# Kernel optimization log

Measured on AMD Instinct MI355X. Metric: run time of the kernel, lower is better.

## Reference

```python
import jax, jax.numpy as jnp
import numpy as np

N = 100_000  # nodes
E = 1_600_000  # edges (before self-loops)
NEG_SLOPE = 0.2  # PyG GATConv default leaky_relu slope


def gat_layer(x, W, a_src, a_dst, b, src, dst, heads, out_ch, concat):
    # x: [N, Fin]; W: [Fin, heads*out_ch]; a_src/a_dst: [1, heads, out_ch]
    h = (x @ W).reshape(-1, heads, out_ch)            # [N, H, C]
    alpha_s = jnp.sum(h * a_src, axis=-1)             # [N, H]
    alpha_d = jnp.sum(h * a_dst, axis=-1)             # [N, H]
    e = jax.nn.leaky_relu(alpha_s[src] + alpha_d[dst], NEG_SLOPE)  # [E', H]
    # softmax over edges grouped by destination node (self-loops guarantee
    # every node has at least one incoming edge)
    m = jax.ops.segment_max(e, dst, num_segments=N)   # [N, H]
    p = jnp.exp(e - m[dst])                           # [E', H]
    s = jax.ops.segment_sum(p, dst, num_segments=N)   # [N, H]
    alpha = p / s[dst]                                # [E', H]
    out = jax.ops.segment_sum(alpha[:, :, None] * h[src], dst, num_segments=N)  # [N,H,C]
    out = out.reshape(-1, heads * out_ch) if concat else out.mean(axis=1)
    return out + b


def setup_inputs() -> dict:
    key = jax.random.key(0)
    ks = jax.random.split(key, 8)

    def glorot(k, shape):
        return (jax.random.normal(k, shape, jnp.float32) / np.sqrt(np.float32(shape[0]))).astype(jnp.float32)

    x = jax.random.normal(ks[0], (N, 512), jnp.float32)
    edge_index = jax.random.randint(ks[1], (2, E), 0, N, dtype=jnp.int64)
    W1 = glorot(ks[2], (512, 64))
    att_src1 = jax.random.normal(ks[3], (1, 8, 8), jnp.float32) * 0.1
    att_dst1 = jax.random.normal(ks[4], (1, 8, 8), jnp.float32) * 0.1
    b1 = jnp.zeros((64,), jnp.float32)
    W2 = glorot(ks[5], (64, 128))
    att_src2 = jax.random.normal(ks[6], (1, 1, 128), jnp.float32) * 0.1
    att_dst2 = jax.random.normal(ks[7], (1, 1, 128), jnp.float32) * 0.1
    b2 = jnp.zeros((128,), jnp.float32)
    return {"x": x, "edge_index": edge_index, "W1": W1, "att_src1": att_src1,
            "att_dst1": att_dst1, "b1": b1, "W2": W2, "att_src2": att_src2,
            "att_dst2": att_dst2, "b2": b2}


def reference(x, edge_index, W1, att_src1, att_dst1, b1, W2, att_src2, att_dst2, b2):
    # PyG GATConv adds self-loops by default
    loop = jnp.arange(N, dtype=edge_index.dtype)
    src = jnp.concatenate([edge_index[0], loop])
    dst = jnp.concatenate([edge_index[1], loop])
    h = gat_layer(x, W1, att_src1, att_dst1, b1, src, dst, heads=8, out_ch=8, concat=True)
    h = jax.nn.elu(h)
    z = gat_layer(h, W2, att_src2, att_dst2, b2, src, dst, heads=1, out_ch=128, concat=False)
    return z
```

## Files before the change

kernel.cpp:

```cpp
#include <hip/hip_runtime.h>
#include <math.h>

#define NNODES 100000

__device__ __forceinline__ float lrelu(float v) { return v > 0.f ? v : 0.2f * v; }

__global__ __launch_bounds__(256) void gemm1_k(const float* __restrict__ x,
                                               const float* __restrict__ W,
                                               float* __restrict__ h1, int Nn) {
    __shared__ float xs[64][132];
    __shared__ float ws[64][68];
    int r0 = blockIdx.x * 128;
    int t = threadIdx.x;
    int ty = t >> 4, tx = t & 15;
    float acc[8][4] = {};
    for (int kb = 0; kb < 512; kb += 64) {
        for (int l = t; l < 2048; l += 256) {
            int row = l >> 4;
            int c4 = (l & 15) * 4;
            int gr = r0 + row;
            float4 v = make_float4(0.f, 0.f, 0.f, 0.f);
            if (gr < Nn) v = *reinterpret_cast<const float4*>(&x[(size_t)gr * 512 + kb + c4]);
            xs[c4][row] = v.x; xs[c4 + 1][row] = v.y; xs[c4 + 2][row] = v.z; xs[c4 + 3][row] = v.w;
        }
        for (int l = t; l < 1024; l += 256) {
            int row = l >> 4;
            int c4 = (l & 15) * 4;
            *reinterpret_cast<float4*>(&ws[row][c4]) =
                *reinterpret_cast<const float4*>(&W[(size_t)(kb + row) * 64 + c4]);
        }
        __syncthreads();
#pragma unroll 4
        for (int k = 0; k < 64; ++k) {
            float4 a0 = *reinterpret_cast<const float4*>(&xs[k][ty * 8]);
            float4 a1 = *reinterpret_cast<const float4*>(&xs[k][ty * 8 + 4]);
            float4 bv = *reinterpret_cast<const float4*>(&ws[k][tx * 4]);
            float a[8] = {a0.x, a0.y, a0.z, a0.w, a1.x, a1.y, a1.z, a1.w};
            float b[4] = {bv.x, bv.y, bv.z, bv.w};
#pragma unroll
            for (int i = 0; i < 8; ++i)
#pragma unroll
                for (int j = 0; j < 4; ++j) acc[i][j] += a[i] * b[j];
        }
        __syncthreads();
    }
#pragma unroll
    for (int i = 0; i < 8; ++i) {
        int gr = r0 + ty * 8 + i;
        if (gr < Nn) {
            float4 o = make_float4(acc[i][0], acc[i][1], acc[i][2], acc[i][3]);
            *reinterpret_cast<float4*>(&h1[(size_t)gr * 64 + tx * 4]) = o;
        }
    }
}

__global__ __launch_bounds__(256) void gemm2_k(const float* __restrict__ xin,
                                               const float* __restrict__ W,
                                               float* __restrict__ h2, int Nn) {
    __shared__ float xs[64][68];
    __shared__ float ws[64][132];
    int r0 = blockIdx.x * 64;
    int t = threadIdx.x;
    int ty = t >> 4, tx = t & 15;
    for (int l = t; l < 1024; l += 256) {
        int row = l >> 4;
        int c4 = (l & 15) * 4;
        int gr = r0 + row;
        float4 v = make_float4(0.f, 0.f, 0.f, 0.f);
        if (gr < Nn) v = *reinterpret_cast<const float4*>(&xin[(size_t)gr * 64 + c4]);
        xs[c4][row] = v.x; xs[c4 + 1][row] = v.y; xs[c4 + 2][row] = v.z; xs[c4 + 3][row] = v.w;
    }
    for (int l = t; l < 2048; l += 256) {
        int row = l >> 5;
        int c4 = (l & 31) * 4;
        *reinterpret_cast<float4*>(&ws[row][c4]) =
            *reinterpret_cast<const float4*>(&W[(size_t)row * 128 + c4]);
    }
    __syncthreads();
    float acc0[4][4] = {};
    float acc1[4][4] = {};
#pragma unroll 4
    for (int k = 0; k < 64; ++k) {
        float4 av = *reinterpret_cast<const float4*>(&xs[k][ty * 4]);
        float4 b0v = *reinterpret_cast<const float4*>(&ws[k][tx * 4]);
        float4 b1v = *reinterpret_cast<const float4*>(&ws[k][64 + tx * 4]);
        float a[4] = {av.x, av.y, av.z, av.w};
        float b0[4] = {b0v.x, b0v.y, b0v.z, b0v.w};
        float b1[4] = {b1v.x, b1v.y, b1v.z, b1v.w};
#pragma unroll
        for (int i = 0; i < 4; ++i)
#pragma unroll
            for (int j = 0; j < 4; ++j) {
                acc0[i][j] += a[i] * b0[j];
                acc1[i][j] += a[i] * b1[j];
            }
    }
#pragma unroll
    for (int i = 0; i < 4; ++i) {
        int gr = r0 + ty * 4 + i;
        if (gr < Nn) {
            float4 o0 = make_float4(acc0[i][0], acc0[i][1], acc0[i][2], acc0[i][3]);
            float4 o1 = make_float4(acc1[i][0], acc1[i][1], acc1[i][2], acc1[i][3]);
            *reinterpret_cast<float4*>(&h2[(size_t)gr * 128 + tx * 4]) = o0;
            *reinterpret_cast<float4*>(&h2[(size_t)gr * 128 + 64 + tx * 4]) = o1;
        }
    }
}

__global__ __launch_bounds__(256) void attn1_k(const float* __restrict__ h1,
                                               const float* __restrict__ asrc,
                                               const float* __restrict__ adst,
                                               float* __restrict__ as1,
                                               float* __restrict__ ad1, int Nn) {
    int t = blockIdx.x * 256 + threadIdx.x;
    int n = t >> 3, h = t & 7;
    if (n >= Nn) return;
    const float* hp = h1 + (size_t)n * 64 + h * 8;
    float s = 0.f, d = 0.f;
#pragma unroll
    for (int c = 0; c < 8; ++c) {
        float v = hp[c];
        s += v * asrc[h * 8 + c];
        d += v * adst[h * 8 + c];
    }
    as1[(size_t)n * 8 + h] = s;
    ad1[(size_t)n * 8 + h] = d;
}

__global__ __launch_bounds__(256) void attn2_k(const float* __restrict__ h2,
                                               const float* __restrict__ asrc,
                                               const float* __restrict__ adst,
                                               float* __restrict__ as2,
                                               float* __restrict__ ad2, int Nn) {
    int wid = threadIdx.x >> 6, lane = threadIdx.x & 63;
    int n = blockIdx.x * 4 + wid;
    if (n >= Nn) return;
    float v0 = h2[(size_t)n * 128 + lane];
    float v1 = h2[(size_t)n * 128 + 64 + lane];
    float s = v0 * asrc[lane] + v1 * asrc[64 + lane];
    float d = v0 * adst[lane] + v1 * adst[64 + lane];
#pragma unroll
    for (int off = 32; off >= 1; off >>= 1) {
        s += __shfl_xor(s, off);
        d += __shfl_xor(d, off);
    }
    if (lane == 0) { as2[n] = s; ad2[n] = d; }
}

__global__ __launch_bounds__(256) void hist_k(const int* __restrict__ ei, int E, int Etot,
                                              int* __restrict__ indeg) {
    int e = blockIdx.x * 256 + threadIdx.x;
    if (e >= Etot) return;
    int d = (e < E) ? ei[E + e] : (e - E);
    atomicAdd(&indeg[d], 1);
}

__global__ __launch_bounds__(256) void scanA_k(const int* __restrict__ indeg,
                                               int* __restrict__ indptr,
                                               int* __restrict__ bsums, int Nn) {
    __shared__ int sd[256];
    int t = threadIdx.x;
    int i0 = blockIdx.x * 2048 + t * 8;
    int v[8], ex[8];
    int run = 0;
#pragma unroll
    for (int j = 0; j < 8; ++j) {
        int i = i0 + j;
        v[j] = (i < Nn) ? indeg[i] : 0;
        ex[j] = run;
        run += v[j];
    }
    sd[t] = run;
    __syncthreads();
    for (int off = 1; off < 256; off <<= 1) {
        int a = (t >= off) ? sd[t - off] : 0;
        __syncthreads();
        sd[t] += a;
        __syncthreads();
    }
    int texc = sd[t] - run;
#pragma unroll
    for (int j = 0; j < 8; ++j) {
        int i = i0 + j;
        if (i < Nn) indptr[i] = texc + ex[j];
    }
    if (t == 0) bsums[blockIdx.x] = sd[255];
}

__global__ void scanB_k(int* __restrict__ bsums, int nb) {
    if (threadIdx.x == 0 && blockIdx.x == 0) {
        int run = 0;
        for (int b = 0; b < nb; ++b) {
            int x = bsums[b];
            bsums[b] = run;
            run += x;
        }
    }
}

__global__ __launch_bounds__(256) void scanC_k(int* __restrict__ indptr,
                                               const int* __restrict__ bsums,
                                               int* __restrict__ cursor, int Nn, int Etot) {
    int t = threadIdx.x;
    int b = blockIdx.x;
    int base = bsums[b];
    int i0 = b * 2048 + t * 8;
#pragma unroll
    for (int j = 0; j < 8; ++j) {
        int i = i0 + j;
        if (i < Nn) {
            int val = indptr[i] + base;
            indptr[i] = val;
            cursor[i] = val;
        }
    }
    if (b == 0 && t == 0) indptr[Nn] = Etot;
}

__global__ __launch_bounds__(256) void fill_k(const int* __restrict__ ei, int E, int Etot,
                                              int* __restrict__ cursor, int* __restrict__ col) {
    int e = blockIdx.x * 256 + threadIdx.x;
    if (e >= Etot) return;
    int s, d;
    if (e < E) { s = ei[e]; d = ei[E + e]; }
    else { s = e - E; d = e - E; }
    int pos = atomicAdd(&cursor[d], 1);
    col[pos] = s;
}

__global__ __launch_bounds__(256) void agg1_k(const float* __restrict__ h1,
                                              const float* __restrict__ as1,
                                              const float* __restrict__ ad1,
                                              const int* __restrict__ indptr,
                                              const int* __restrict__ col,
                                              const float* __restrict__ b1,
                                              float* __restrict__ h1a, int Nn) {
    int wid = threadIdx.x >> 6, lane = threadIdx.x & 63;
    int n = blockIdx.x * 4 + wid;
    if (n >= Nn) return;
    int beg = indptr[n], end = indptr[n + 1];
    int h = lane & 7, eo = lane >> 3;
    float adn = ad1[(size_t)n * 8 + h];
    float ss = 0.f;
    for (int i = beg + eo; i < end; i += 8) {
        int s = col[i];
        ss += __expf(lrelu(as1[(size_t)s * 8 + h] + adn));
    }
    ss += __shfl_xor(ss, 8);
    ss += __shfl_xor(ss, 16);
    ss += __shfl_xor(ss, 32);
    int hb = lane >> 3;
    float sb = __shfl(ss, hb);
    float ab = __shfl(adn, hb);
    float inv = 1.f / sb;
    const float* __restrict__ h1l = h1 + lane;
    float acc0 = 0.f, acc1 = 0.f, acc2 = 0.f, acc3 = 0.f;
    int i = beg;
    for (; i + 4 <= end; i += 4) {
        int s0 = col[i], s1 = col[i + 1], s2 = col[i + 2], s3 = col[i + 3];
        float w0 = __expf(lrelu(as1[(size_t)s0 * 8 + hb] + ab));
        float w1 = __expf(lrelu(as1[(size_t)s1 * 8 + hb] + ab));
        float w2 = __expf(lrelu(as1[(size_t)s2 * 8 + hb] + ab));
        float w3 = __expf(lrelu(as1[(size_t)s3 * 8 + hb] + ab));
        acc0 += w0 * h1l[(size_t)s0 * 64];
        acc1 += w1 * h1l[(size_t)s1 * 64];
        acc2 += w2 * h1l[(size_t)s2 * 64];
        acc3 += w3 * h1l[(size_t)s3 * 64];
    }
    for (; i < end; ++i) {
        int s = col[i];
        acc0 += __expf(lrelu(as1[(size_t)s * 8 + hb] + ab)) * h1l[(size_t)s * 64];
    }
    float o = ((acc0 + acc1) + (acc2 + acc3)) * inv + b1[lane];
    h1a[(size_t)n * 64 + lane] = o > 0.f ? o : expm1f(o);
}

__global__ __launch_bounds__(256) void agg2_k(const float* __restrict__ h2,
                                              const float* __restrict__ as2,
                                              const float* __restrict__ ad2,
                                              const int* __restrict__ indptr,
                                              const int* __restrict__ col,
                                              const float* __restrict__ b2,
                                              float* __restrict__ out, int Nn) {
    int wid = threadIdx.x >> 6, lane = threadIdx.x & 63;
    int n = blockIdx.x * 4 + wid;
    if (n >= Nn) return;
    int beg = indptr[n], end = indptr[n + 1];
    float adn = ad2[n];
    float ss = 0.f;
    for (int i = beg + lane; i < end; i += 64) {
        ss += __expf(lrelu(as2[col[i]] + adn));
    }
#pragma unroll
    for (int off = 32; off >= 1; off >>= 1) ss += __shfl_xor(ss, off);
    float inv = 1.f / ss;
    const float* __restrict__ h2l = h2 + lane;
    float a00 = 0.f, a01 = 0.f, a02 = 0.f, a03 = 0.f;
    float a10 = 0.f, a11 = 0.f, a12 = 0.f, a13 = 0.f;
    int i = beg;
    for (; i + 4 <= end; i += 4) {
        int s0 = col[i], s1 = col[i + 1], s2 = col[i + 2], s3 = col[i + 3];
        float w0 = __expf(lrelu(as2[s0] + adn));
        float w1 = __expf(lrelu(as2[s1] + adn));
        float w2 = __expf(lrelu(as2[s2] + adn));
        float w3 = __expf(lrelu(as2[s3] + adn));
        a00 += w0 * h2l[(size_t)s0 * 128];
        a10 += w0 * h2l[(size_t)s0 * 128 + 64];
        a01 += w1 * h2l[(size_t)s1 * 128];
        a11 += w1 * h2l[(size_t)s1 * 128 + 64];
        a02 += w2 * h2l[(size_t)s2 * 128];
        a12 += w2 * h2l[(size_t)s2 * 128 + 64];
        a03 += w3 * h2l[(size_t)s3 * 128];
        a13 += w3 * h2l[(size_t)s3 * 128 + 64];
    }
    for (; i < end; ++i) {
        int s = col[i];
        float w = __expf(lrelu(as2[s] + adn));
        a00 += w * h2l[(size_t)s * 128];
        a10 += w * h2l[(size_t)s * 128 + 64];
    }
    out[(size_t)n * 128 + lane] = ((a00 + a01) + (a02 + a03)) * inv + b2[lane];
    out[(size_t)n * 128 + 64 + lane] = ((a10 + a11) + (a12 + a13)) * inv + b2[64 + lane];
}

extern "C" void kernel_launch(void* const* d_in, const int* in_sizes, int n_in,
                              void* d_out, int out_size, void* d_ws, size_t ws_size,
                              hipStream_t stream) {
    const float* x = (const float*)d_in[0];
    const int* ei = (const int*)d_in[1];
    const float* W1 = (const float*)d_in[2];
    const float* asrc1 = (const float*)d_in[3];
    const float* adst1 = (const float*)d_in[4];
    const float* b1 = (const float*)d_in[5];
    const float* W2 = (const float*)d_in[6];
    const float* asrc2 = (const float*)d_in[7];
    const float* adst2 = (const float*)d_in[8];
    const float* b2 = (const float*)d_in[9];
    float* out = (float*)d_out;

    const int Nn = NNODES;
    const int E = in_sizes[1] / 2;
    const int Etot = E + Nn;

    char* w = (char*)d_ws;
    auto alloc = [&](size_t bytes) {
        char* p = w;
        w += (bytes + 255) & ~(size_t)255;
        return p;
    };
    float* h1 = (float*)alloc((size_t)Nn * 64 * 4);
    float* h1a = (float*)alloc((size_t)Nn * 64 * 4);
    float* h2 = (float*)alloc((size_t)Nn * 128 * 4);
    float* as1 = (float*)alloc((size_t)Nn * 8 * 4);
    float* ad1 = (float*)alloc((size_t)Nn * 8 * 4);
    float* as2 = (float*)alloc((size_t)Nn * 4);
    float* ad2 = (float*)alloc((size_t)Nn * 4);
    int* indeg = (int*)alloc((size_t)(Nn + 1) * 4);
    int* indptr = (int*)alloc((size_t)(Nn + 1) * 4);
    int* cursor = (int*)alloc((size_t)Nn * 4);
    int* bsums = (int*)alloc(4096);
    int* col = (int*)alloc((size_t)Etot * 4);

    const int NBLK = (Nn + 2047) / 2048;

    hipMemsetAsync(indeg, 0, (size_t)Nn * 4, stream);
    gemm1_k<<<(Nn + 127) / 128, 256, 0, stream>>>(x, W1, h1, Nn);
    attn1_k<<<(Nn * 8 + 255) / 256, 256, 0, stream>>>(h1, asrc1, adst1, as1, ad1, Nn);
    hist_k<<<(Etot + 255) / 256, 256, 0, stream>>>(ei, E, Etot, indeg);
    scanA_k<<<NBLK, 256, 0, stream>>>(indeg, indptr, bsums, Nn);
    scanB_k<<<1, 64, 0, stream>>>(bsums, NBLK);
    scanC_k<<<NBLK, 256, 0, stream>>>(indptr, bsums, cursor, Nn, Etot);
    fill_k<<<(Etot + 255) / 256, 256, 0, stream>>>(ei, E, Etot, cursor, col);
    agg1_k<<<(Nn + 3) / 4, 256, 0, stream>>>(h1, as1, ad1, indptr, col, b1, h1a, Nn);
    gemm2_k<<<(Nn + 63) / 64, 256, 0, stream>>>(h1a, W2, h2, Nn);
    attn2_k<<<(Nn + 3) / 4, 256, 0, stream>>>(h2, asrc2, adst2, as2, ad2, Nn);
    agg2_k<<<(Nn + 3) / 4, 256, 0, stream>>>(h2, as2, ad2, indptr, col, b2, out, Nn);
}
```

Measured before the change: 877.9 us.

## Retile both GEMMs with swizzled row-major LDS and unroll aggregation loops by eight

The x and hidden tiles are now stored row-major in LDS with an XOR swizzle, which replaces the transposed scalar stores. Each thread now computes an 8x8 output tile, and gemm1 runs with 128 threads per block while gemm2 handles 128 rows per block. The two edge-aggregation kernels unroll their gather loop from four to eight edges, keeping more independent loads in flight. This adds register pressure, which could lower occupancy, and the larger gemm2 blocks reduce the number of blocks launched.

Result: slower. 1.010 ms (+15.0%).

```diff
diff --git a/kernel.cpp b/kernel.cpp
--- a/kernel.cpp
+++ b/kernel.cpp
@@ -5,104 +5,133 @@
 
 __device__ __forceinline__ float lrelu(float v) { return v > 0.f ? v : 0.2f * v; }
 
-__global__ __launch_bounds__(256) void gemm1_k(const float* __restrict__ x,
+#define SWZ(row) ((((row) & 3) ^ (((row) >> 3) & 7)) << 2)
+
+__global__ __launch_bounds__(128) void gemm1_k(const float* __restrict__ x,
                                                const float* __restrict__ W,
                                                float* __restrict__ h1, int Nn) {
-    __shared__ float xs[64][132];
-    __shared__ float ws[64][68];
+    __shared__ float xs[128][64];
+    __shared__ float ws[64][64];
+    int r0 = blockIdx.x * 128;
+    int t = threadIdx.x;
+    int ty = t >> 3, tx = t & 7;
+    float acc0[8][4] = {};
+    float acc1[8][4] = {};
+    for (int kb = 0; kb < 512; kb += 64) {
+        for (int l = t; l < 2048; l += 128) {
+            int row = l >> 4;
+            int c4 = (l & 15) << 2;
+            int gr = r0 + row;
+            float4 v = make_float4(0.f, 0.f, 0.f, 0.f);
+            if (gr < Nn) v = *reinterpret_cast<const float4*>(&x[(size_t)gr * 512 + kb + c4]);
+            *reinterpret_cast<float4*>(&xs[row][c4 ^ SWZ(row)]) = v;
+        }
+        for (int l = t; l < 1024; l += 128) {
+            int row = l >> 4;
+            int c4 = (l & 15) << 2;
+            *reinterpret_cast<float4*>(&ws[row][c4]) =
+                *reinterpret_cast<const float4*>(&W[(size_t)(kb + row) * 64 + c4]);
+        }
+        __syncthreads();
+#pragma unroll 1
+        for (int k0 = 0; k0 < 64; k0 += 4) {
+            float4 av[8];
+#pragma unroll
+            for (int i = 0; i < 8; ++i) {
+                int row = ty * 8 + i;
+                av[i] = *reinterpret_cast<const float4*>(&xs[row][k0 ^ SWZ(row)]);
+            }
+            float4 b0[4], b1[4];
+#pragma unroll
+            for (int kk = 0; kk < 4; ++kk) {
+                b0[kk] = *reinterpret_cast<const float4*>(&ws[k0 + kk][tx * 4]);
+                b1[kk] = *reinterpret_cast<const float4*>(&ws[k0 + kk][32 + tx * 4]);
+            }
+#pragma unroll
+            for (int kk = 0; kk < 4; ++kk) {
+#pragma unroll
+                for (int i = 0; i < 8; ++i) {
+                    float a = (kk == 0) ? av[i].x : (kk == 1) ? av[i].y : (kk == 2) ? av[i].z : av[i].w;
+                    acc0[i][0] += a * b0[kk].x; acc0[i][1] += a * b0[kk].y;
+                    acc0[i][2] += a * b0[kk].z; acc0[i][3] += a * b0[kk].w;
+                    acc1[i][0] += a * b1[kk].x; acc1[i][1] += a * b1[kk].y;
+                    acc1[i][2] += a * b1[kk].z; acc1[i][3] += a * b1[kk].w;
+                }
+            }
+        }
+        __syncthreads();
+    }
+#pragma unroll
+    for (int i = 0; i < 8; ++i) {
+        int gr = r0 + ty * 8 + i;
+        if (gr < Nn) {
+            *reinterpret_cast<float4*>(&h1[(size_t)gr * 64 + tx * 4]) =
+                make_float4(acc0[i][0], acc0[i][1], acc0[i][2], acc0[i][3]);
+            *reinterpret_cast<float4*>(&h1[(size_t)gr * 64 + 32 + tx * 4]) =
+                make_float4(acc1[i][0], acc1[i][1], acc1[i][2], acc1[i][3]);
+        }
+    }
+}
+
+__global__ __launch_bounds__(256) void gemm2_k(const float* __restrict__ xin,
+                                               const float* __restrict__ W,
+                                               float* __restrict__ h2, int Nn) {
+    __shared__ float xs[128][64];
+    __shared__ float ws[64][128];
     int r0 = blockIdx.x * 128;
     int t = threadIdx.x;
     int ty = t >> 4, tx = t & 15;
-    float acc[8][4] = {};
-    for (int kb = 0; kb < 512; kb += 64) {
-        for (int l = t; l < 2048; l += 256) {
-            int row = l >> 4;
-            int c4 = (l & 15) * 4;
-            int gr = r0 + row;
-            float4 v = make_float4(0.f, 0.f, 0.f, 0.f);
-            if (gr < Nn) v = *reinterpret_cast<const float4*>(&x[(size_t)gr * 512 + kb + c4]);
-            xs[c4][row] = v.x; xs[c4 + 1][row] = v.y; xs[c4 + 2][row] = v.z; xs[c4 + 3][row] = v.w;
-        }
-        for (int l = t; l < 1024; l += 256) {
-            int row = l >> 4;
-            int c4 = (l & 15) * 4;
-            *reinterpret_cast<float4*>(&ws[row][c4]) =
-                *reinterpret_cast<const float4*>(&W[(size_t)(kb + row) * 64 + c4]);
-        }
-        __syncthreads();
-#pragma unroll 4
-        for (int k = 0; k < 64; ++k) {
-            float4 a0 = *reinterpret_cast<const float4*>(&xs[k][ty * 8]);
-            float4 a1 = *reinterpret_cast<const float4*>(&xs[k][ty * 8 + 4]);
-            float4 bv = *reinterpret_cast<const float4*>(&ws[k][tx * 4]);
-            float a[8] = {a0.x, a0.y, a0.z, a0.w, a1.x, a1.y, a1.z, a1.w};
-            float b[4] = {bv.x, bv.y, bv.z, bv.w};
-#pragma unroll
-            for (int i = 0; i < 8; ++i)
-#pragma unroll
-                for (int j = 0; j < 4; ++j) acc[i][j] += a[i] * b[j];
-        }
-        __syncthreads();
+    for (int l = t; l < 2048; l += 256) {
+        int row = l >> 4;
+        int c4 = (l & 15) << 2;
+        int gr = r0 + row;
+        float4 v = make_float4(0.f, 0.f, 0.f, 0.f);
+        if (gr < Nn) v = *reinterpret_cast<const float4*>(&xin[(size_t)gr * 64 + c4]);
+        *reinterpret_cast<float4*>(&xs[row][c4 ^ SWZ(row)]) = v;
+    }
+    for (int l = t; l < 2048; l += 256) {
+        int row = l >> 5;
+        int c4 = (l & 31) << 2;
+        *reinterpret_cast<float4*>(&ws[row][c4]) =
+            *reinterpret_cast<const float4*>(&W[(size_t)row * 128 + c4]);
+    }
+    __syncthreads();
+    float acc0[8][4] = {};
+    float acc1[8][4] = {};
+#pragma unroll 1
+    for (int k0 = 0; k0 < 64; k0 += 4) {
+        float4 av[8];
+#pragma unroll
+        for (int i = 0; i < 8; ++i) {
+            int row = ty * 8 + i;
+            av[i] = *reinterpret_cast<const float4*>(&xs[row][k0 ^ SWZ(row)]);
+        }
+        float4 b0[4], b1[4];
+#pragma unroll
+        for (int kk = 0; kk < 4; ++kk) {
+            b0[kk] = *reinterpret_cast<const float4*>(&ws[k0 + kk][tx * 4]);
+            b1[kk] = *reinterpret_cast<const float4*>(&ws[k0 + kk][64 + tx * 4]);
+        }
+#pragma unroll
+        for (int kk = 0; kk < 4; ++kk) {
+#pragma unroll
+            for (int i = 0; i < 8; ++i) {
+                float a = (kk == 0) ? av[i].x : (kk == 1) ? av[i].y : (kk == 2) ? av[i].z : av[i].w;
+                acc0[i][0] += a * b0[kk].x; acc0[i][1] += a * b0[kk].y;
+                acc0[i][2] += a * b0[kk].z; acc0[i][3] += a * b0[kk].w;
+                acc1[i][0] += a * b1[kk].x; acc1[i][1] += a * b1[kk].y;
+                acc1[i][2] += a * b1[kk].z; acc1[i][3] += a * b1[kk].w;
+            }
+        }
     }
 #pragma unroll
     for (int i = 0; i < 8; ++i) {
         int gr = r0 + ty * 8 + i;
         if (gr < Nn) {
-            float4 o = make_float4(acc[i][0], acc[i][1], acc[i][2], acc[i][3]);
-            *reinterpret_cast<float4*>(&h1[(size_t)gr * 64 + tx * 4]) = o;
-        }
-    }
-}
-
-__global__ __launch_bounds__(256) void gemm2_k(const float* __restrict__ xin,
-                                               const float* __restrict__ W,
-                                               float* __restrict__ h2, int Nn) {
-    __shared__ float xs[64][68];
-    __shared__ float ws[64][132];
-    int r0 = blockIdx.x * 64;
-    int t = threadIdx.x;
-    int ty = t >> 4, tx = t & 15;
-    for (int l = t; l < 1024; l += 256) {
-        int row = l >> 4;
-        int c4 = (l & 15) * 4;
-        int gr = r0 + row;
-        float4 v = make_float4(0.f, 0.f, 0.f, 0.f);
-        if (gr < Nn) v = *reinterpret_cast<const float4*>(&xin[(size_t)gr * 64 + c4]);
-        xs[c4][row] = v.x; xs[c4 + 1][row] = v.y; xs[c4 + 2][row] = v.z; xs[c4 + 3][row] = v.w;
-    }
-    for (int l = t; l < 2048; l += 256) {
-        int row = l >> 5;
-        int c4 = (l & 31) * 4;
-        *reinterpret_cast<float4*>(&ws[row][c4]) =
-            *reinterpret_cast<const float4*>(&W[(size_t)row * 128 + c4]);
-    }
-    __syncthreads();
-    float acc0[4][4] = {};
-    float acc1[4][4] = {};
-#pragma unroll 4
-    for (int k = 0; k < 64; ++k) {
-        float4 av = *reinterpret_cast<const float4*>(&xs[k][ty * 4]);
-        float4 b0v = *reinterpret_cast<const float4*>(&ws[k][tx * 4]);
-        float4 b1v = *reinterpret_cast<const float4*>(&ws[k][64 + tx * 4]);
-        float a[4] = {av.x, av.y, av.z, av.w};
-        float b0[4] = {b0v.x, b0v.y, b0v.z, b0v.w};
-        float b1[4] = {b1v.x, b1v.y, b1v.z, b1v.w};
-#pragma unroll
-        for (int i = 0; i < 4; ++i)
-#pragma unroll
-            for (int j = 0; j < 4; ++j) {
-                acc0[i][j] += a[i] * b0[j];
-                acc1[i][j] += a[i] * b1[j];
-            }
-    }
-#pragma unroll
-    for (int i = 0; i < 4; ++i) {
-        int gr = r0 + ty * 4 + i;
-        if (gr < Nn) {
-            float4 o0 = make_float4(acc0[i][0], acc0[i][1], acc0[i][2], acc0[i][3]);
-            float4 o1 = make_float4(acc1[i][0], acc1[i][1], acc1[i][2], acc1[i][3]);
-            *reinterpret_cast<float4*>(&h2[(size_t)gr * 128 + tx * 4]) = o0;
-            *reinterpret_cast<float4*>(&h2[(size_t)gr * 128 + 64 + tx * 4]) = o1;
+            *reinterpret_cast<float4*>(&h2[(size_t)gr * 128 + tx * 4]) =
+                make_float4(acc0[i][0], acc0[i][1], acc0[i][2], acc0[i][3]);
+            *reinterpret_cast<float4*>(&h2[(size_t)gr * 128 + 64 + tx * 4]) =
+                make_float4(acc1[i][0], acc1[i][1], acc1[i][2], acc1[i][3]);
         }
     }
 }
@@ -255,23 +284,33 @@
     float inv = 1.f / sb;
     const float* __restrict__ h1l = h1 + lane;
     float acc0 = 0.f, acc1 = 0.f, acc2 = 0.f, acc3 = 0.f;
+    float acc4 = 0.f, acc5 = 0.f, acc6 = 0.f, acc7 = 0.f;
     int i = beg;
-    for (; i + 4 <= end; i += 4) {
+    for (; i + 8 <= end; i += 8) {
         int s0 = col[i], s1 = col[i + 1], s2 = col[i + 2], s3 = col[i + 3];
+        int s4 = col[i + 4], s5 = col[i + 5], s6 = col[i + 6], s7 = col[i + 7];
         float w0 = __expf(lrelu(as1[(size_t)s0 * 8 + hb] + ab));
         float w1 = __expf(lrelu(as1[(size_t)s1 * 8 + hb] + ab));
         float w2 = __expf(lrelu(as1[(size_t)s2 * 8 + hb] + ab));
         float w3 = __expf(lrelu(as1[(size_t)s3 * 8 + hb] + ab));
+        float w4 = __expf(lrelu(as1[(size_t)s4 * 8 + hb] + ab));
+        float w5 = __expf(lrelu(as1[(size_t)s5 * 8 + hb] + ab));
+        float w6 = __expf(lrelu(as1[(size_t)s6 * 8 + hb] + ab));
+        float w7 = __expf(lrelu(as1[(size_t)s7 * 8 + hb] + ab));
         acc0 += w0 * h1l[(size_t)s0 * 64];
         acc1 += w1 * h1l[(size_t)s1 * 64];
         acc2 += w2 * h1l[(size_t)s2 * 64];
         acc3 += w3 * h1l[(size_t)s3 * 64];
+        acc4 += w4 * h1l[(size_t)s4 * 64];
+        acc5 += w5 * h1l[(size_t)s5 * 64];
+        acc6 += w6 * h1l[(size_t)s6 * 64];
+        acc7 += w7 * h1l[(size_t)s7 * 64];
     }
     for (; i < end; ++i) {
         int s = col[i];
         acc0 += __expf(lrelu(as1[(size_t)s * 8 + hb] + ab)) * h1l[(size_t)s * 64];
     }
-    float o = ((acc0 + acc1) + (acc2 + acc3)) * inv + b1[lane];
+    float o = (((acc0 + acc1) + (acc2 + acc3)) + ((acc4 + acc5) + (acc6 + acc7))) * inv + b1[lane];
     h1a[(size_t)n * 64 + lane] = o > 0.f ? o : expm1f(o);
 }
 
@@ -296,22 +335,29 @@
     float inv = 1.f / ss;
     const float* __restrict__ h2l = h2 + lane;
     float a00 = 0.f, a01 = 0.f, a02 = 0.f, a03 = 0.f;
+    float a04 = 0.f, a05 = 0.f, a06 = 0.f, a07 = 0.f;
     float a10 = 0.f, a11 = 0.f, a12 = 0.f, a13 = 0.f;
+    float a14 = 0.f, a15 = 0.f, a16 = 0.f, a17 = 0.f;
     int i = beg;
-    for (; i + 4 <= end; i += 4) {
+    for (; i + 8 <= end; i += 8) {
         int s0 = col[i], s1 = col[i + 1], s2 = col[i + 2], s3 = col[i + 3];
+        int s4 = col[i + 4], s5 = col[i + 5], s6 = col[i + 6], s7 = col[i + 7];
         float w0 = __expf(lrelu(as2[s0] + adn));
         float w1 = __expf(lrelu(as2[s1] + adn));
         float w2 = __expf(lrelu(as2[s2] + adn));
         float w3 = __expf(lrelu(as2[s3] + adn));
-        a00 += w0 * h2l[(size_t)s0 * 128];
-        a10 += w0 * h2l[(size_t)s0 * 128 + 64];
-        a01 += w1 * h2l[(size_t)s1 * 128];
-        a11 += w1 * h2l[(size_t)s1 * 128 + 64];
-        a02 += w2 * h2l[(size_t)s2 * 128];
-        a12 += w2 * h2l[(size_t)s2 * 128 + 64];
-        a03 += w3 * h2l[(size_t)s3 * 128];
-        a13 += w3 * h2l[(size_t)s3 * 128 + 64];
+        float w4 = __expf(lrelu(as2[s4] + adn));
+        float w5 = __expf(lrelu(as2[s5] + adn));
+        float w6 = __expf(lrelu(as2[s6] + adn));
+        float w7 = __expf(lrelu(as2[s7] + adn));
+        a00 += w0 * h2l[(size_t)s0 * 128]; a10 += w0 * h2l[(size_t)s0 * 128 + 64];
+        a01 += w1 * h2l[(size_t)s1 * 128]; a11 += w1 * h2l[(size_t)s1 * 128 + 64];
+        a02 += w2 * h2l[(size_t)s2 * 128]; a12 += w2 * h2l[(size_t)s2 * 128 + 64];
+        a03 += w3 * h2l[(size_t)s3 * 128]; a13 += w3 * h2l[(size_t)s3 * 128 + 64];
+        a04 += w4 * h2l[(size_t)s4 * 128]; a14 += w4 * h2l[(size_t)s4 * 128 + 64];
+        a05 += w5 * h2l[(size_t)s5 * 128]; a15 += w5 * h2l[(size_t)s5 * 128 + 64];
+        a06 += w6 * h2l[(size_t)s6 * 128]; a16 += w6 * h2l[(size_t)s6 * 128 + 64];
+        a07 += w7 * h2l[(size_t)s7 * 128]; a17 += w7 * h2l[(size_t)s7 * 128 + 64];
     }
     for (; i < end; ++i) {
         int s = col[i];
@@ -319,8 +365,10 @@
         a00 += w * h2l[(size_t)s * 128];
         a10 += w * h2l[(size_t)s * 128 + 64];
     }
-    out[(size_t)n * 128 + lane] = ((a00 + a01) + (a02 + a03)) * inv + b2[lane];
-    out[(size_t)n * 128 + 64 + lane] = ((a10 + a11) + (a12 + a13)) * inv + b2[64 + lane];
+    float r0 = ((a00 + a01) + (a02 + a03)) + ((a04 + a05) + (a06 + a07));
+    float r1 = ((a10 + a11) + (a12 + a13)) + ((a14 + a15) + (a16 + a17));
+    out[(size_t)n * 128 + lane] = r0 * inv + b2[lane];
+    out[(size_t)n * 128 + 64 + lane] = r1 * inv + b2[64 + lane];
 }
 
 extern "C" void kernel_launch(void* const* d_in, const int* in_sizes, int n_in,
@@ -364,7 +412,7 @@
     const int NBLK = (Nn + 2047) / 2048;
 
     hipMemsetAsync(indeg, 0, (size_t)Nn * 4, stream);
-    gemm1_k<<<(Nn + 127) / 128, 256, 0, stream>>>(x, W1, h1, Nn);
+    gemm1_k<<<(Nn + 127) / 128, 128, 0, stream>>>(x, W1, h1, Nn);
     attn1_k<<<(Nn * 8 + 255) / 256, 256, 0, stream>>>(h1, asrc1, adst1, as1, ad1, Nn);
     hist_k<<<(Etot + 255) / 256, 256, 0, stream>>>(ei, E, Etot, indeg);
     scanA_k<<<NBLK, 256, 0, stream>>>(indeg, indptr, bsums, Nn);
@@ -372,7 +420,7 @@
     scanC_k<<<NBLK, 256, 0, stream>>>(indptr, bsums, cursor, Nn, Etot);
     fill_k<<<(Etot + 255) / 256, 256, 0, stream>>>(ei, E, Etot, cursor, col);
     agg1_k<<<(Nn + 3) / 4, 256, 0, stream>>>(h1, as1, ad1, indptr, col, b1, h1a, Nn);
-    gemm2_k<<<(Nn + 63) / 64, 256, 0, stream>>>(h1a, W2, h2, Nn);
+    gemm2_k<<<(Nn + 127) / 128, 256, 0, stream>>>(h1a, W2, h2, Nn);
     attn2_k<<<(Nn + 3) / 4, 256, 0, stream>>>(h2, asrc2, adst2, as2, ad2, Nn);
     agg2_k<<<(Nn + 3) / 4, 256, 0, stream>>>(h2, as2, ad2, indptr, col, b2, out, Nn);
 }
```
